# Performance work log

Measured on AMD Instinct MI355X. Metric: run time of the kernel, lower is better.

The kernel has to match this reference:

```python
import jax, jax.numpy as jnp
import numpy as np

N_NODES = 20000
N_EDGES = 1280000
IN_CH = 256
HID_CH = 256


def setup_inputs() -> dict:
    key = jax.random.key(0)
    ks = jax.random.split(key, 8)
    s = 1.0 / np.sqrt(IN_CH)
    sh = 1.0 / np.sqrt(HID_CH)
    return {
        "x": jax.random.normal(ks[0], (N_NODES, IN_CH), dtype=jnp.float32),
        "edge_index": jax.random.randint(ks[1], (2, N_EDGES), 0, N_NODES, dtype=jnp.int64),
        "W1_l": jax.random.normal(ks[2], (HID_CH, IN_CH), dtype=jnp.float32) * s,
        "b1": jnp.zeros((HID_CH,), dtype=jnp.float32),
        "W1_r": jax.random.normal(ks[3], (HID_CH, IN_CH), dtype=jnp.float32) * s,
        "W2_l": jax.random.normal(ks[4], (1, HID_CH), dtype=jnp.float32) * sh,
        "b2": jnp.zeros((1,), dtype=jnp.float32),
        "W2_r": jax.random.normal(ks[5], (1, HID_CH), dtype=jnp.float32) * sh,
        "fc_w": jax.random.normal(ks[6], (1, N_NODES), dtype=jnp.float32) * (1.0 / np.sqrt(N_NODES)),
        "fc_b": jnp.zeros((1,), dtype=jnp.float32),
    }


def _sage(x, src, dst, inv_deg, W_l, b, W_r):
    # mean-aggregate source features at destination nodes, then two linears
    agg = jax.ops.segment_sum(x[src], dst, num_segments=N_NODES)  # [N, C]
    mean = agg * inv_deg[:, None]
    return mean @ W_l.T + b + x @ W_r.T


def reference(x, edge_index, W1_l, b1, W1_r, W2_l, b2, W2_r, fc_w, fc_b):
    src, dst = edge_index[0], edge_index[1]
    deg = jax.ops.segment_sum(jnp.ones((dst.shape[0],), dtype=x.dtype), dst,
                              num_segments=N_NODES)
    inv_deg = 1.0 / jnp.maximum(deg, 1.0)  # isolated nodes -> 0 aggregate
    h = jax.nn.relu(_sage(x, src, dst, inv_deg, W1_l, b1, W1_r))   # [N, H]
    h = jax.nn.relu(_sage(h, src, dst, inv_deg, W2_l, b2, W2_r))   # [N, 1]
    h = h[:, 0]                                                     # squeeze dim 1
    return h @ fc_w[0] + fc_b                                       # [1]
```

## Files before the change

### kernel.cpp

```cpp
#include <hip/hip_runtime.h>

#define N_NODESC 20000
#define N_EDGESC 1280000
#define NB 256
#define EPB 5000

typedef short bf16x8 __attribute__((ext_vector_type(8)));
typedef float f32x4 __attribute__((ext_vector_type(4)));

constexpr size_t OFF_DEG      = 0;
constexpr size_t OFF_ROWSTART = 81920;
constexpr size_t OFF_INVDEG   = 163840;
constexpr size_t OFF_BSUM     = 245760;
constexpr size_t OFF_BOFF     = 246272;
constexpr size_t OFF_S1       = 246784;
constexpr size_t OFF_T1       = 326784;
constexpr size_t OFF_PART     = 406784;
constexpr size_t OFF_HIST     = 427264;
constexpr size_t OFF_CSR      = 10667264;
constexpr size_t OFF_XB       = 13227392;
constexpr size_t OFF_MEANB    = 23467392;
constexpr size_t OFF_W1LB     = 33707392;
constexpr size_t OFF_W1RB     = 33838464;

static __device__ __forceinline__ unsigned f2bf(float f) {
    unsigned u = __float_as_uint(f);
    return ((u + 0x7fffu + ((u >> 16) & 1u)) >> 16) & 0xffffu;
}
static __device__ __forceinline__ float bflo(unsigned w) {
    return __uint_as_float(w << 16);
}
static __device__ __forceinline__ float bfhi(unsigned w) {
    return __uint_as_float(w & 0xffff0000u);
}

__global__ void __launch_bounds__(256) k_cast(
        const float4* __restrict__ x, const float4* __restrict__ w1l,
        const float4* __restrict__ w1r, uint4* __restrict__ xb,
        uint4* __restrict__ w1lb, uint4* __restrict__ w1rb,
        float* __restrict__ s1, float* __restrict__ t1,
        int* __restrict__ bsum) {
    int g = blockIdx.x * 256 + threadIdx.x;
    if (g < N_NODESC) { s1[g] = 0.0f; t1[g] = 0.0f; }
    if (g < 128) bsum[g] = 0;
    const float4* src; uint4* dst; int off;
    if (g < 640000)      { src = x;   dst = xb;   off = g; }
    else if (g < 648192) { src = w1l; dst = w1lb; off = g - 640000; }
    else                 { src = w1r; dst = w1rb; off = g - 648192; }
    float4 a = src[off * 2], b = src[off * 2 + 1];
    uint4 o;
    o.x = f2bf(a.x) | (f2bf(a.y) << 16);
    o.y = f2bf(a.z) | (f2bf(a.w) << 16);
    o.z = f2bf(b.x) | (f2bf(b.y) << 16);
    o.w = f2bf(b.z) | (f2bf(b.w) << 16);
    dst[off] = o;
}

__global__ void __launch_bounds__(256) k_hist(const int* __restrict__ ei,
                                              unsigned short* __restrict__ hist) {
    __shared__ unsigned int lh[10000];
    int b = blockIdx.x, t = threadIdx.x;
    for (int w = t; w < 10000; w += 256) lh[w] = 0;
    __syncthreads();
    int base = b * EPB;
    for (int i = t; i < EPB; i += 256) {
        int d = ei[N_EDGESC + base + i];
        atomicAdd(&lh[d >> 1], (d & 1) ? 0x10000u : 1u);
    }
    __syncthreads();
    unsigned int* gh = (unsigned int*)(hist + (size_t)b * N_NODESC);
    for (int w = t; w < 10000; w += 256) gh[w] = lh[w];
}

__global__ void __launch_bounds__(256) k_prefix(unsigned short* __restrict__ hist,
                                                int* __restrict__ deg,
                                                int* __restrict__ bsum) {
    __shared__ int wtot[4][64];
    int t = threadIdx.x;
    int lb = t & 63, sub = t >> 6;
    int bin = blockIdx.x * 64 + lb;
    bool ok = bin < N_NODESC;
    int vals[64];
    int run = 0;
    if (ok) {
        #pragma unroll
        for (int i = 0; i < 64; i++) {
            vals[i] = hist[(size_t)(sub * 64 + i) * N_NODESC + bin];
            run += vals[i];
        }
    }
    wtot[sub][lb] = run;
    __syncthreads();
    int off = 0, total = 0;
    for (int w = 0; w < 4; w++) {
        int v = wtot[w][lb];
        if (w < sub) off += v;
        total += v;
    }
    if (sub == 0) {
        int tv = ok ? total : 0;
        if (ok) deg[bin] = total;
        #pragma unroll
        for (int o2 = 32; o2 > 0; o2 >>= 1) tv += __shfl_down(tv, o2);
        if (lb == 0) atomicAdd(&bsum[(blockIdx.x * 64) >> 8], tv);
    }
    if (ok) {
        int run2 = off;
        #pragma unroll
        for (int i = 0; i < 64; i++) {
            hist[(size_t)(sub * 64 + i) * N_NODESC + bin] = (unsigned short)run2;
            run2 += vals[i];
        }
    }
}

__global__ void k_scan2(const int* __restrict__ bsum, int* __restrict__ boff,
                        int* __restrict__ row_start) {
    __shared__ int sm[128];
    int t = threadIdx.x;
    int v = (t < 79) ? bsum[t] : 0;
    sm[t] = v;
    __syncthreads();
    for (int off = 1; off < 128; off <<= 1) {
        int add = (t >= off) ? sm[t - off] : 0;
        __syncthreads();
        sm[t] += add;
        __syncthreads();
    }
    if (t < 79) boff[t] = sm[t] - v;
    if (t == 0) row_start[N_NODESC] = sm[127];
}

__global__ void __launch_bounds__(256) k_scan3(
        const int* __restrict__ deg, const int* __restrict__ boff,
        int* __restrict__ row_start, float* __restrict__ inv_deg) {
    __shared__ int wsum[4];
    int i = blockIdx.x * 256 + threadIdx.x;
    int lane = threadIdx.x & 63, wid = threadIdx.x >> 6;
    int v = (i < N_NODESC) ? deg[i] : 0;
    int incl = v;
    #pragma unroll
    for (int off = 1; off < 64; off <<= 1) {
        int n = __shfl_up(incl, off);
        if (lane >= off) incl += n;
    }
    if (lane == 63) wsum[wid] = incl;
    __syncthreads();
    int wpre = 0;
    #pragma unroll
    for (int w = 0; w < 4; w++) wpre += (w < wid) ? wsum[w] : 0;
    if (i < N_NODESC) {
        row_start[i] = boff[blockIdx.x] + wpre + incl - v;
        inv_deg[i]   = 1.0f / (float)max(v, 1);
    }
}

__global__ void __launch_bounds__(256) k_fill2(const int* __restrict__ ei,
        const int* __restrict__ row_start, const unsigned short* __restrict__ hist,
        unsigned short* __restrict__ csr) {
    __shared__ unsigned int lh[10000];
    int b = blockIdx.x, t = threadIdx.x;
    for (int w = t; w < 10000; w += 256) lh[w] = 0;
    __syncthreads();
    int base = b * EPB;
    const unsigned short* hb = hist + (size_t)b * N_NODESC;
    for (int i = t; i < EPB; i += 256) {
        int e = base + i;
        int d = ei[N_EDGESC + e];
        int s = ei[e];
        unsigned int old = atomicAdd(&lh[d >> 1], (d & 1) ? 0x10000u : 1u);
        int rank = (d & 1) ? (int)(old >> 16) : (int)(old & 0xffffu);
        int pos = row_start[d] + (int)hb[d] + rank;
        csr[pos] = (unsigned short)s;
    }
}

__global__ void __launch_bounds__(256) k_agg(const char* __restrict__ xbc,
        const int* __restrict__ row_start, const unsigned short* __restrict__ csr,
        const float* __restrict__ inv_deg, uint4* __restrict__ meanb4) {
    int wid = threadIdx.x >> 6, lane = threadIdx.x & 63;
    int node = blockIdx.x * 4 + wid;
    int pass = blockIdx.y;
    int ol = lane & 7, oct = lane >> 3;
    unsigned lanebyte = ((unsigned)(pass << 3) + (unsigned)ol) << 4;
    int start = row_start[node], end = row_start[node + 1];
    float a0=0.f,a1=0.f,a2=0.f,a3=0.f,a4=0.f,a5=0.f,a6=0.f,a7=0.f;
    float c0=0.f,c1=0.f,c2=0.f,c3=0.f,c4=0.f,c5=0.f,c6=0.f,c7=0.f;
    int idx = (start < end) ? (int)csr[start + lane] : 0;
    for (int j = start; j < end; j += 64) {
        int cnt = min(64, end - j);
        int idxn = (j + 64 < end) ? (int)csr[j + 64 + lane] : 0;
        int fs = cnt >> 3;
        int k = 0;
        for (; k + 2 <= fs; k += 2) {
            int s0 = __shfl(idx, 8 * k + oct);
            int s1 = __shfl(idx, 8 * k + 8 + oct);
            uint4 v0 = *(const uint4*)(xbc + (((unsigned)s0 << 9) + lanebyte));
            uint4 v1 = *(const uint4*)(xbc + (((unsigned)s1 << 9) + lanebyte));
            a0 += bflo(v0.x); a1 += bfhi(v0.x); a2 += bflo(v0.y); a3 += bfhi(v0.y);
            a4 += bflo(v0.z); a5 += bfhi(v0.z); a6 += bflo(v0.w); a7 += bfhi(v0.w);
            c0 += bflo(v1.x); c1 += bfhi(v1.x); c2 += bflo(v1.y); c3 += bfhi(v1.y);
            c4 += bflo(v1.z); c5 += bfhi(v1.z); c6 += bflo(v1.w); c7 += bfhi(v1.w);
        }
        if (k < fs) {
            int s0 = __shfl(idx, 8 * k + oct);
            uint4 v = *(const uint4*)(xbc + (((unsigned)s0 << 9) + lanebyte));
            a0 += bflo(v.x); a1 += bfhi(v.x); a2 += bflo(v.y); a3 += bfhi(v.y);
            a4 += bflo(v.z); a5 += bfhi(v.z); a6 += bflo(v.w); a7 += bfhi(v.w);
        }
        int rem = cnt & 7;
        if (rem) {
            int s0 = __shfl(idx, 8 * fs + oct);
            if (oct < rem) {
                uint4 v = *(const uint4*)(xbc + (((unsigned)s0 << 9) + lanebyte));
                c0 += bflo(v.x); c1 += bfhi(v.x); c2 += bflo(v.y); c3 += bfhi(v.y);
                c4 += bflo(v.z); c5 += bfhi(v.z); c6 += bflo(v.w); c7 += bfhi(v.w);
            }
        }
        idx = idxn;
    }
    a0 += c0; a1 += c1; a2 += c2; a3 += c3;
    a4 += c4; a5 += c5; a6 += c6; a7 += c7;
    a0 += __shfl_down(a0, 32); a1 += __shfl_down(a1, 32);
    a2 += __shfl_down(a2, 32); a3 += __shfl_down(a3, 32);
    a4 += __shfl_down(a4, 32); a5 += __shfl_down(a5, 32);
    a6 += __shfl_down(a6, 32); a7 += __shfl_down(a7, 32);
    a0 += __shfl_down(a0, 16); a1 += __shfl_down(a1, 16);
    a2 += __shfl_down(a2, 16); a3 += __shfl_down(a3, 16);
    a4 += __shfl_down(a4, 16); a5 += __shfl_down(a5, 16);
    a6 += __shfl_down(a6, 16); a7 += __shfl_down(a7, 16);
    a0 += __shfl_down(a0, 8);  a1 += __shfl_down(a1, 8);
    a2 += __shfl_down(a2, 8);  a3 += __shfl_down(a3, 8);
    a4 += __shfl_down(a4, 8);  a5 += __shfl_down(a5, 8);
    a6 += __shfl_down(a6, 8);  a7 += __shfl_down(a7, 8);
    if (oct == 0) {
        float inv = inv_deg[node];
        uint4 o;
        o.x = f2bf(a0 * inv) | (f2bf(a1 * inv) << 16);
        o.y = f2bf(a2 * inv) | (f2bf(a3 * inv) << 16);
        o.z = f2bf(a4 * inv) | (f2bf(a5 * inv) << 16);
        o.w = f2bf(a6 * inv) | (f2bf(a7 * inv) << 16);
        meanb4[(size_t)node * 32 + (pass << 3) + ol] = o;
    }
}

__global__ void __launch_bounds__(256) k_gemm(const uint4* __restrict__ meanb4,
        const uint4* __restrict__ xb4, const uint4* __restrict__ w1lb4,
        const uint4* __restrict__ w1rb4, const float* __restrict__ b1,
        const float* __restrict__ w2l, const float* __restrict__ w2r,
        float* __restrict__ s1, float* __restrict__ t1) {
    __shared__ __align__(16) unsigned short As[32][72];
    __shared__ __align__(16) unsigned short Bs[256][72];
    int t = threadIdx.x;
    int m0 = blockIdx.x * 32;
    int wv = t >> 6, l = t & 63, lr = l & 15, quad = l >> 4;
    int mh = wv & 1;
    int nh = wv >> 1;
    f32x4 acc[8] = {{0,0,0,0},{0,0,0,0},{0,0,0,0},{0,0,0,0},
                    {0,0,0,0},{0,0,0,0},{0,0,0,0},{0,0,0,0}};
    for (int kt = 0; kt < 8; kt++) {
        const uint4* Asrc = (kt < 4) ? meanb4 : xb4;
        const uint4* Bsrc = (kt < 4) ? w1lb4 : w1rb4;
        int k0q = (kt & 3) * 8;
        {
            int row = t >> 3, cc = t & 7;
            uint4 va = Asrc[(size_t)(m0 + row) * 32 + k0q + cc];
            *(uint4*)&As[row][cc * 8] = va;
        }
        #pragma unroll
        for (int p = 0; p < 8; p++) {
            int f = p * 256 + t;
            int row = f >> 3, cc = f & 7;
            uint4 vb = Bsrc[(size_t)row * 32 + k0q + cc];
            *(uint4*)&Bs[row][cc * 8] = vb;
        }
        __syncthreads();
        #pragma unroll
        for (int ks = 0; ks < 64; ks += 32) {
            bf16x8 af = *(const bf16x8*)&As[mh * 16 + lr][ks + quad * 8];
            #pragma unroll
            for (int g = 0; g < 8; g++) {
                bf16x8 bf = *(const bf16x8*)&Bs[(nh * 8 + g) * 16 + lr][ks + quad * 8];
                acc[g] = __builtin_amdgcn_mfma_f32_16x16x32_bf16(
                             af, bf, acc[g], 0, 0, 0);
            }
        }
        __syncthreads();
    }
    float ps[4] = {0, 0, 0, 0}, pt[4] = {0, 0, 0, 0};
    #pragma unroll
    for (int g = 0; g < 8; g++) {
        int col = (nh * 8 + g) * 16 + lr;
        float bb = b1[col], wl = w2l[col], wr = w2r[col];
        #pragma unroll
        for (int r = 0; r < 4; r++) {
            float h = fmaxf(acc[g][r] + bb, 0.0f);
            ps[r] += h * wl; pt[r] += h * wr;
        }
    }
    #pragma unroll
    for (int r = 0; r < 4; r++) {
        #pragma unroll
        for (int off = 8; off > 0; off >>= 1) {
            ps[r] += __shfl_down(ps[r], off, 16);
            pt[r] += __shfl_down(pt[r], off, 16);
        }
    }
    if (lr == 0) {
        int mb = m0 + mh * 16 + quad * 4;
        #pragma unroll
        for (int r = 0; r < 4; r++) {
            int m = mb + r;
            atomicAdd(&s1[m], ps[r]);
            atomicAdd(&t1[m], pt[r]);
        }
    }
}

__global__ void __launch_bounds__(256) k_layer2(
        const int* __restrict__ row_start, const unsigned short* __restrict__ csr,
        const float* __restrict__ inv_deg, const float* __restrict__ s1,
        const float* __restrict__ t1, const float* __restrict__ b2,
        const float* __restrict__ fc_w, float* __restrict__ part) {
    __shared__ float pw[4];
    int wid = threadIdx.x >> 6, lane = threadIdx.x & 63;
    int node = blockIdx.x * 4 + wid;
    float contrib = 0.0f;
    if (node < N_NODESC) {
        int start = row_start[node], end = row_start[node + 1];
        float s = 0.0f;
        for (int j = start + lane; j < end; j += 64) s += s1[csr[j]];
        #pragma unroll
        for (int off = 32; off > 0; off >>= 1) s += __shfl_down(s, off);
        if (lane == 0) {
            float h2 = fmaxf(s * inv_deg[node] + b2[0] + t1[node], 0.0f);
            contrib = h2 * fc_w[node];
        }
    }
    if (lane == 0) pw[wid] = contrib;
    __syncthreads();
    if (threadIdx.x == 0)
        part[blockIdx.x] = pw[0] + pw[1] + pw[2] + pw[3];
}

__global__ void __launch_bounds__(256) k_final(const float* __restrict__ part,
        const float* __restrict__ fc_b, float* __restrict__ out) {
    __shared__ float sm[4];
    int t = threadIdx.x;
    float s = 0.0f;
    for (int i = t; i < 5000; i += 256) s += part[i];
    #pragma unroll
    for (int off = 32; off > 0; off >>= 1) s += __shfl_down(s, off);
    if ((t & 63) == 0) sm[t >> 6] = s;
    __syncthreads();
    if (t == 0) out[0] = sm[0] + sm[1] + sm[2] + sm[3] + fc_b[0];
}

extern "C" void kernel_launch(void* const* d_in, const int* in_sizes, int n_in,
                              void* d_out, int out_size, void* d_ws, size_t ws_size,
                              hipStream_t stream) {
    const float* x    = (const float*)d_in[0];
    const int*   ei   = (const int*)d_in[1];
    const float* w1l  = (const float*)d_in[2];
    const float* b1   = (const float*)d_in[3];
    const float* w1r  = (const float*)d_in[4];
    const float* w2l  = (const float*)d_in[5];
    const float* b2   = (const float*)d_in[6];
    const float* w2r  = (const float*)d_in[7];
    const float* fcw  = (const float*)d_in[8];
    const float* fcb  = (const float*)d_in[9];
    float* out = (float*)d_out;

    char* ws = (char*)d_ws;
    int*    deg       = (int*)(ws + OFF_DEG);
    int*    row_start = (int*)(ws + OFF_ROWSTART);
    float*  inv_deg   = (float*)(ws + OFF_INVDEG);
    int*    bsum      = (int*)(ws + OFF_BSUM);
    int*    boff      = (int*)(ws + OFF_BOFF);
    float*  s1        = (float*)(ws + OFF_S1);
    float*  t1        = (float*)(ws + OFF_T1);
    float*  part      = (float*)(ws + OFF_PART);
    unsigned short* hist = (unsigned short*)(ws + OFF_HIST);
    unsigned short* csr  = (unsigned short*)(ws + OFF_CSR);
    char*   xbc       = (char*)(ws + OFF_XB);
    uint4*  meanb4    = (uint4*)(ws + OFF_MEANB);
    uint4*  w1lb4     = (uint4*)(ws + OFF_W1LB);
    uint4*  w1rb4     = (uint4*)(ws + OFF_W1RB);

    k_cast<<<2564, 256, 0, stream>>>((const float4*)x, (const float4*)w1l,
                                     (const float4*)w1r, (uint4*)xbc,
                                     w1lb4, w1rb4, s1, t1, bsum);
    k_hist<<<NB, 256, 0, stream>>>(ei, hist);
    k_prefix<<<313, 256, 0, stream>>>(hist, deg, bsum);
    k_scan2<<<1, 128, 0, stream>>>(bsum, boff, row_start);
    k_scan3<<<79, 256, 0, stream>>>(deg, boff, row_start, inv_deg);
    k_fill2<<<NB, 256, 0, stream>>>(ei, row_start, hist, csr);
    dim3 agrid(5000, 4);
    k_agg<<<agrid, 256, 0, stream>>>(xbc, row_start, csr, inv_deg, meanb4);
    k_gemm<<<625, 256, 0, stream>>>(meanb4, (const uint4*)xbc,
                                    w1lb4, w1rb4, b1, w2l, w2r, s1, t1);
    k_layer2<<<5000, 256, 0, stream>>>(row_start, csr, inv_deg, s1, t1, b2,
                                       fcw, part);
    k_final<<<1, 256, 0, stream>>>(part, fcb, out);
}
```

Measured before the change: 216.8 us.

## Fuse cast with histogram, drop separate scan kernel, halve edge-partition block count

The bf16 cast and the per-block destination histogram now run in one launch, with extra blocks appended for the histogram work. The separate single-block scan over block sums is removed: each k_scan3 block reduces the preceding block sums itself, and the final row_start entry is written as the known edge count. The edge partitioning drops from 256 to 128 blocks of 10000 edges, and k_prefix is adjusted to match. This cuts two kernel launches and halves the histogram traffic. In exchange, the cast blocks now reserve 40KB of LDS, which can lower their occupancy, and the fill phase has fewer blocks to run in parallel.

After: 222.7 us. 2.7% more time.

```diff
diff --git a/kernel.cpp b/kernel.cpp
--- a/kernel.cpp
+++ b/kernel.cpp
@@ -2,8 +2,9 @@
 
 #define N_NODESC 20000
 #define N_EDGESC 1280000
-#define NB 256
-#define EPB 5000
+#define NB 128
+#define EPB 10000
+#define CASTB 2564
 
 typedef short bf16x8 __attribute__((ext_vector_type(8)));
 typedef float f32x4 __attribute__((ext_vector_type(4)));
@@ -12,7 +13,6 @@
 constexpr size_t OFF_ROWSTART = 81920;
 constexpr size_t OFF_INVDEG   = 163840;
 constexpr size_t OFF_BSUM     = 245760;
-constexpr size_t OFF_BOFF     = 246272;
 constexpr size_t OFF_S1       = 246784;
 constexpr size_t OFF_T1       = 326784;
 constexpr size_t OFF_PART     = 406784;
@@ -34,12 +34,28 @@
     return __uint_as_float(w & 0xffff0000u);
 }
 
-__global__ void __launch_bounds__(256) k_cast(
+__global__ void __launch_bounds__(256) k_cast_hist(
         const float4* __restrict__ x, const float4* __restrict__ w1l,
         const float4* __restrict__ w1r, uint4* __restrict__ xb,
         uint4* __restrict__ w1lb, uint4* __restrict__ w1rb,
         float* __restrict__ s1, float* __restrict__ t1,
-        int* __restrict__ bsum) {
+        int* __restrict__ bsum,
+        const int* __restrict__ ei, unsigned short* __restrict__ hist) {
+    __shared__ unsigned int lh[10000];
+    if (blockIdx.x >= CASTB) {
+        int b = blockIdx.x - CASTB, t = threadIdx.x;
+        for (int w = t; w < 10000; w += 256) lh[w] = 0;
+        __syncthreads();
+        int base = b * EPB;
+        for (int i = t; i < EPB; i += 256) {
+            int d = ei[N_EDGESC + base + i];
+            atomicAdd(&lh[d >> 1], (d & 1) ? 0x10000u : 1u);
+        }
+        __syncthreads();
+        unsigned int* gh = (unsigned int*)(hist + (size_t)b * N_NODESC);
+        for (int w = t; w < 10000; w += 256) gh[w] = lh[w];
+        return;
+    }
     int g = blockIdx.x * 256 + threadIdx.x;
     if (g < N_NODESC) { s1[g] = 0.0f; t1[g] = 0.0f; }
     if (g < 128) bsum[g] = 0;
@@ -56,22 +72,6 @@
     dst[off] = o;
 }
 
-__global__ void __launch_bounds__(256) k_hist(const int* __restrict__ ei,
-                                              unsigned short* __restrict__ hist) {
-    __shared__ unsigned int lh[10000];
-    int b = blockIdx.x, t = threadIdx.x;
-    for (int w = t; w < 10000; w += 256) lh[w] = 0;
-    __syncthreads();
-    int base = b * EPB;
-    for (int i = t; i < EPB; i += 256) {
-        int d = ei[N_EDGESC + base + i];
-        atomicAdd(&lh[d >> 1], (d & 1) ? 0x10000u : 1u);
-    }
-    __syncthreads();
-    unsigned int* gh = (unsigned int*)(hist + (size_t)b * N_NODESC);
-    for (int w = t; w < 10000; w += 256) gh[w] = lh[w];
-}
-
 __global__ void __launch_bounds__(256) k_prefix(unsigned short* __restrict__ hist,
                                                 int* __restrict__ deg,
                                                 int* __restrict__ bsum) {
@@ -80,12 +80,12 @@
     int lb = t & 63, sub = t >> 6;
     int bin = blockIdx.x * 64 + lb;
     bool ok = bin < N_NODESC;
-    int vals[64];
+    int vals[32];
     int run = 0;
     if (ok) {
         #pragma unroll
-        for (int i = 0; i < 64; i++) {
-            vals[i] = hist[(size_t)(sub * 64 + i) * N_NODESC + bin];
+        for (int i = 0; i < 32; i++) {
+            vals[i] = hist[(size_t)(sub * 32 + i) * N_NODESC + bin];
             run += vals[i];
         }
     }
@@ -107,36 +107,25 @@
     if (ok) {
         int run2 = off;
         #pragma unroll
-        for (int i = 0; i < 64; i++) {
-            hist[(size_t)(sub * 64 + i) * N_NODESC + bin] = (unsigned short)run2;
+        for (int i = 0; i < 32; i++) {
+            hist[(size_t)(sub * 32 + i) * N_NODESC + bin] = (unsigned short)run2;
             run2 += vals[i];
         }
     }
 }
 
-__global__ void k_scan2(const int* __restrict__ bsum, int* __restrict__ boff,
-                        int* __restrict__ row_start) {
-    __shared__ int sm[128];
-    int t = threadIdx.x;
-    int v = (t < 79) ? bsum[t] : 0;
-    sm[t] = v;
-    __syncthreads();
-    for (int off = 1; off < 128; off <<= 1) {
-        int add = (t >= off) ? sm[t - off] : 0;
-        __syncthreads();
-        sm[t] += add;
-        __syncthreads();
-    }
-    if (t < 79) boff[t] = sm[t] - v;
-    if (t == 0) row_start[N_NODESC] = sm[127];
-}
-
 __global__ void __launch_bounds__(256) k_scan3(
-        const int* __restrict__ deg, const int* __restrict__ boff,
+        const int* __restrict__ deg, const int* __restrict__ bsum,
         int* __restrict__ row_start, float* __restrict__ inv_deg) {
     __shared__ int wsum[4];
+    __shared__ int bb[4];
     int i = blockIdx.x * 256 + threadIdx.x;
-    int lane = threadIdx.x & 63, wid = threadIdx.x >> 6;
+    int t = threadIdx.x;
+    int lane = t & 63, wid = t >> 6;
+    int bv = (t < (int)blockIdx.x) ? bsum[t] : 0;
+    #pragma unroll
+    for (int off = 32; off > 0; off >>= 1) bv += __shfl_down(bv, off);
+    if (lane == 0) bb[wid] = bv;
     int v = (i < N_NODESC) ? deg[i] : 0;
     int incl = v;
     #pragma unroll
@@ -146,13 +135,15 @@
     }
     if (lane == 63) wsum[wid] = incl;
     __syncthreads();
+    int boffv = bb[0] + bb[1] + bb[2] + bb[3];
     int wpre = 0;
     #pragma unroll
     for (int w = 0; w < 4; w++) wpre += (w < wid) ? wsum[w] : 0;
     if (i < N_NODESC) {
-        row_start[i] = boff[blockIdx.x] + wpre + incl - v;
+        row_start[i] = boffv + wpre + incl - v;
         inv_deg[i]   = 1.0f / (float)max(v, 1);
     }
+    if (blockIdx.x == 0 && t == 0) row_start[N_NODESC] = N_EDGESC;
 }
 
 __global__ void __launch_bounds__(256) k_fill2(const int* __restrict__ ei,
@@ -376,7 +367,6 @@
     int*    row_start = (int*)(ws + OFF_ROWSTART);
     float*  inv_deg   = (float*)(ws + OFF_INVDEG);
     int*    bsum      = (int*)(ws + OFF_BSUM);
-    int*    boff      = (int*)(ws + OFF_BOFF);
     float*  s1        = (float*)(ws + OFF_S1);
     float*  t1        = (float*)(ws + OFF_T1);
     float*  part      = (float*)(ws + OFF_PART);
@@ -387,13 +377,11 @@
     uint4*  w1lb4     = (uint4*)(ws + OFF_W1LB);
     uint4*  w1rb4     = (uint4*)(ws + OFF_W1RB);
 
-    k_cast<<<2564, 256, 0, stream>>>((const float4*)x, (const float4*)w1l,
-                                     (const float4*)w1r, (uint4*)xbc,
-                                     w1lb4, w1rb4, s1, t1, bsum);
-    k_hist<<<NB, 256, 0, stream>>>(ei, hist);
+    k_cast_hist<<<CASTB + NB, 256, 0, stream>>>(
+        (const float4*)x, (const float4*)w1l, (const float4*)w1r,
+        (uint4*)xbc, w1lb4, w1rb4, s1, t1, bsum, ei, hist);
     k_prefix<<<313, 256, 0, stream>>>(hist, deg, bsum);
-    k_scan2<<<1, 128, 0, stream>>>(bsum, boff, row_start);
-    k_scan3<<<79, 256, 0, stream>>>(deg, boff, row_start, inv_deg);
+    k_scan3<<<79, 256, 0, stream>>>(deg, bsum, row_start, inv_deg);
     k_fill2<<<NB, 256, 0, stream>>>(ei, row_start, hist, csr);
     dim3 agrid(5000, 4);
     k_agg<<<agrid, 256, 0, stream>>>(xbc, row_start, csr, inv_deg, meanb4);
```
